# Kernel tuning notes

Hardware: AMD Instinct MI355X
Metric: run time of the kernel (lower is better)

Reference implementation:

```python
import jax, jax.numpy as jnp
import numpy as np

T, B, N, D, O = 500, 64, 512, 100, 10
ALPHA = 0.1


def setup_inputs() -> dict:
    key = jax.random.key(0)
    ks = jax.random.split(key, 13)
    sN = 1.0 / np.sqrt(N)
    sD = 1.0 / np.sqrt(D)
    return {
        "X": jax.random.normal(ks[0], (T, B, D), jnp.float32),
        "W_rec_m1": jax.random.normal(ks[1], (N, N), jnp.float32) * sN,
        "W_rec_pmd": jax.random.normal(ks[2], (N, N), jnp.float32) * sN,
        "W_rec_s1": jax.random.normal(ks[3], (N, N), jnp.float32) * sN,
        "b_m1": jnp.zeros((N,), jnp.float32),
        "b_pmd": jnp.zeros((N,), jnp.float32),
        "b_s1": jnp.zeros((N,), jnp.float32),
        "W_pmd_m1": jax.random.normal(ks[4], (N, N), jnp.float32) * sN,
        "W_s1_m1": jax.random.normal(ks[5], (N, N), jnp.float32) * sN,
        "W_m1_pmd": jax.random.normal(ks[6], (N, N), jnp.float32) * sN,
        "W_in_pmd": jax.random.normal(ks[7], (N, D), jnp.float32) * sD,
        "W_in_s1": jax.random.normal(ks[8], (N, D), jnp.float32) * sD,
        "W_out": jax.random.normal(ks[9], (O, N), jnp.float32) * sN,
    }


def reference(X, W_rec_m1, W_rec_pmd, W_rec_s1, b_m1, b_pmd, b_s1,
              W_pmd_m1, W_s1_m1, W_m1_pmd, W_in_pmd, W_in_s1, W_out):
    a = jnp.float32(ALPHA)

    def step(carry, Xt):
        x_m1, x_pmd, x_s1, r_m1, r_pmd, r_s1 = carry
        # message passing: accumulate inputs to each region
        in_m1 = r_pmd @ W_pmd_m1.T + r_s1 @ W_s1_m1.T            # [B, N]
        in_pmd = r_m1 @ W_m1_pmd.T + Xt @ W_in_pmd.T             # [B, N]
        in_s1 = Xt @ W_in_s1.T                                   # [B, N]
        # leaky-RNN f_step per region
        x_m1 = (1 - a) * x_m1 + a * (r_m1 @ W_rec_m1.T + in_m1 + b_m1)
        x_pmd = (1 - a) * x_pmd + a * (r_pmd @ W_rec_pmd.T + in_pmd + b_pmd)
        x_s1 = (1 - a) * x_s1 + a * (r_s1 @ W_rec_s1.T + in_s1 + b_s1)
        r_m1, r_pmd, r_s1 = jnp.tanh(x_m1), jnp.tanh(x_pmd), jnp.tanh(x_s1)
        out_t = r_m1 @ W_out.T                                   # [B, O]
        return (x_m1, x_pmd, x_s1, r_m1, r_pmd, r_s1), (out_t, r_m1, r_pmd, r_s1)

    z = jnp.zeros((B, N), X.dtype)
    init = (z, z, z, z, z, z)  # zero hidden; rates[0] = tanh(0) = 0
    _, (out, r_m1, r_pmd, r_s1) = jax.lax.scan(step, init, X[1:])
    return out  # [T-1, B, O]
```

## Files before the change

kernel.cpp:

```cpp
#include <hip/hip_runtime.h>
#include <hip/hip_cooperative_groups.h>

namespace cg = cooperative_groups;

#define NT 499
#define NB 64
#define NN 512
#define ND 100
#define NO 10
#define NWAVE 16
#define KW 32
#define NWG 256

typedef float f32x2 __attribute__((ext_vector_type(2)));

#define XT_SZ   (NT * ND * NB)
#define RBUF_SZ (2 * NN * NB)
#define XT_OFF  0
#define RM_OFF  (XT_OFF + XT_SZ)
#define RP_OFF  (RM_OFF + RBUF_SZ)
#define RS_OFF  (RP_OFF + RBUF_SZ)
#define FLAG_OFF (RS_OFF + RBUF_SZ)
#define RPK_STRIDE ((NN / 2) * NB)

__device__ __forceinline__ void st_cg_u(unsigned* p, unsigned v) {
  __hip_atomic_store(p, v, __ATOMIC_RELAXED, __HIP_MEMORY_SCOPE_AGENT);
}

#define LD1(dst, base, voff, IMM) \
  asm volatile("global_load_dword %0, %1, %2 offset:" IMM " sc0 sc1" \
               : "=v"(dst) : "v"(voff), "s"(base))
#define LDR(u, base, voff) do { \
  LD1(u[0],  base, voff, "0");    LD1(u[1],  base, voff, "256");  \
  LD1(u[2],  base, voff, "512");  LD1(u[3],  base, voff, "768");  \
  LD1(u[4],  base, voff, "1024"); LD1(u[5],  base, voff, "1280"); \
  LD1(u[6],  base, voff, "1536"); LD1(u[7],  base, voff, "1792"); \
  LD1(u[8],  base, voff, "2048"); LD1(u[9],  base, voff, "2304"); \
  LD1(u[10], base, voff, "2560"); LD1(u[11], base, voff, "2816"); \
  LD1(u[12], base, voff, "3072"); LD1(u[13], base, voff, "3328"); \
  LD1(u[14], base, voff, "3584"); LD1(u[15], base, voff, "3840"); \
} while (0)

#define LD_SC(dst, addr) \
  asm volatile("global_load_dword %0, %1, off sc0 sc1" : "=v"(dst) : "v"(addr))

#define PKFMA(acc, a, w) \
  asm("v_pk_fma_f32 %0, %1, %2, %0" : "+v"(acc) : "v"(a), "s"(w))

__device__ __forceinline__ unsigned f2bf(float f) {
  unsigned u = __float_as_uint(f);
  return (u + 0x7fffu + ((u >> 16) & 1u)) >> 16;
}

__global__ void xpose_kernel(const float* __restrict__ X, float* __restrict__ XT) {
  __shared__ float tile[NB * ND];
  const int t = blockIdx.x;
  const float* src = X + (size_t)(t + 1) * NB * ND;
  for (int i = threadIdx.x; i < NB * ND; i += blockDim.x) tile[i] = src[i];
  __syncthreads();
  float* dst = XT + (size_t)t * ND * NB;
  for (int i = threadIdx.x; i < NB * ND; i += blockDim.x) {
    const int d = i >> 6, b = i & 63;
    dst[i] = tile[b * ND + d];
  }
}

__global__ void __launch_bounds__(1024, 4)
rnn_kernel(const float* __restrict__ XT,
           unsigned* __restrict__ rmPK, unsigned* __restrict__ rpPK,
           unsigned* __restrict__ rsPK,
           const float* __restrict__ W_rec_m1, const float* __restrict__ W_rec_pmd,
           const float* __restrict__ W_rec_s1,
           const float* __restrict__ b_m1, const float* __restrict__ b_pmd,
           const float* __restrict__ b_s1,
           const float* __restrict__ W_pmd_m1, const float* __restrict__ W_s1_m1,
           const float* __restrict__ W_m1_pmd, const float* __restrict__ W_in_pmd,
           const float* __restrict__ W_in_s1, const float* __restrict__ W_out,
           float* __restrict__ out,
           unsigned* __restrict__ flags, unsigned* __restrict__ gen)
{
  (void)gen;
  const int g    = blockIdx.x;
  const int grp  = g >> 4;
  const int wave = __builtin_amdgcn_readfirstlane((int)threadIdx.x >> 6);
  const int lane = (int)threadIdx.x & 63;
  const int n0 = 2 * g, n1 = 2 * g + 1;
  const int k0 = __builtin_amdgcn_readfirstlane(wave * KW);
  const int m0 = __builtin_amdgcn_readfirstlane(wave * (KW / 2));
  const int d0 = __builtin_amdgcn_readfirstlane(wave * 7);
  int dlen = ND - d0; dlen = dlen < 0 ? 0 : (dlen > 7 ? 7 : dlen);
  const bool has_out = (g < NO);
  const unsigned voff = (unsigned)lane * 4u;

  __shared__ float red[NWAVE][7][64];

  for (int i = g * (int)blockDim.x + (int)threadIdx.x; i < RPK_STRIDE;
       i += (int)(gridDim.x * blockDim.x)) {
    rmPK[i] = 0u; rpPK[i] = 0u; rsPK[i] = 0u;
  }
  if (g <= 16 && threadIdx.x == 0) flags[g * 16] = 0u;

  const float* wrm0 = W_rec_m1 + (size_t)n0 * NN + k0;
  const float* wrm1 = W_rec_m1 + (size_t)n1 * NN + k0;
  const float* wmp0 = W_m1_pmd + (size_t)n0 * NN + k0;
  const float* wmp1 = W_m1_pmd + (size_t)n1 * NN + k0;
  const float* wpm0 = W_pmd_m1 + (size_t)n0 * NN + k0;
  const float* wpm1 = W_pmd_m1 + (size_t)n1 * NN + k0;
  const float* wrp0 = W_rec_pmd + (size_t)n0 * NN + k0;
  const float* wrp1 = W_rec_pmd + (size_t)n1 * NN + k0;
  const float* wsm0 = W_s1_m1 + (size_t)n0 * NN + k0;
  const float* wsm1 = W_s1_m1 + (size_t)n1 * NN + k0;
  const float* wrs0 = W_rec_s1 + (size_t)n0 * NN + k0;
  const float* wrs1 = W_rec_s1 + (size_t)n1 * NN + k0;
  const float* wip0 = W_in_pmd + (size_t)n0 * ND + d0;
  const float* wip1 = W_in_pmd + (size_t)n1 * ND + d0;
  const float* wis0 = W_in_s1 + (size_t)n0 * ND + d0;
  const float* wis1 = W_in_s1 + (size_t)n1 * ND + d0;
  const float* wo   = W_out + (size_t)(has_out ? g : 0) * NN + k0;

  unsigned* pubPK = nullptr; float bP0 = 0.f, bP1 = 0.f;
  if (wave == 0)      { pubPK = rmPK; bP0 = b_m1[n0];  bP1 = b_m1[n1]; }
  else if (wave == 1) { pubPK = rpPK; bP0 = b_pmd[n0]; bP1 = b_pmd[n1]; }
  else if (wave == 2) { pubPK = rsPK; bP0 = b_s1[n0];  bP1 = b_s1[n1]; }
  float xP0 = 0.f, xP1 = 0.f;

  float apX0 = 0.f, apX1 = 0.f, asX0 = 0.f, asX1 = 0.f;
  {
    const float* xt = XT + d0 * NB + lane;
    for (int d = 0; d < dlen; ++d) {
      const float v = xt[d * NB];
      apX0 = fmaf(v, wip0[d], apX0);
      apX1 = fmaf(v, wip1[d], apX1);
      asX0 = fmaf(v, wis0[d], asX0);
      asX1 = fmaf(v, wis1[d], asX1);
    }
  }

  cg::this_grid().sync();

  for (int ti = 0; ti < NT; ++ti) {
    const int cur = ti & 1, nxt = cur ^ 1;
    const unsigned* bM = rmPK + cur * RPK_STRIDE + m0 * NB;
    const unsigned* bP = rpPK + cur * RPK_STRIDE + m0 * NB;
    const unsigned* bS = rsPK + cur * RPK_STRIDE + m0 * NB;

    unsigned um[16], uP[16], uS[16];
    LDR(um, bM, voff);
    LDR(uP, bP, voff);
    LDR(uS, bS, voff);
    asm volatile("s_waitcnt vmcnt(0)" ::: "memory");
    __builtin_amdgcn_sched_barrier(0);

    f32x2 vm2[16];
    #pragma unroll
    for (int j = 0; j < 16; ++j) {
      vm2[j].x = __uint_as_float(um[j] << 16);
      vm2[j].y = __uint_as_float(um[j] & 0xffff0000u);
    }

    f32x2 am0p = {0.f, 0.f}, am1p = {0.f, 0.f};
    f32x2 ap0p = {apX0, 0.f}, ap1p = {apX1, 0.f};
    f32x2 as0p = {asX0, 0.f}, as1p = {asX1, 0.f};

    #pragma unroll
    for (int j = 0; j < 16; ++j) {
      const f32x2 w0 = *(const f32x2*)(wrm0 + 2 * j);
      const f32x2 w1 = *(const f32x2*)(wrm1 + 2 * j);
      const f32x2 w2 = *(const f32x2*)(wmp0 + 2 * j);
      const f32x2 w3 = *(const f32x2*)(wmp1 + 2 * j);
      PKFMA(am0p, vm2[j], w0);
      PKFMA(am1p, vm2[j], w1);
      PKFMA(ap0p, vm2[j], w2);
      PKFMA(ap1p, vm2[j], w3);
    }
    #pragma unroll
    for (int j = 0; j < 16; ++j) {
      f32x2 v; v.x = __uint_as_float(uP[j] << 16);
               v.y = __uint_as_float(uP[j] & 0xffff0000u);
      const f32x2 w0 = *(const f32x2*)(wpm0 + 2 * j);
      const f32x2 w1 = *(const f32x2*)(wpm1 + 2 * j);
      const f32x2 w2 = *(const f32x2*)(wrp0 + 2 * j);
      const f32x2 w3 = *(const f32x2*)(wrp1 + 2 * j);
      PKFMA(am0p, v, w0);
      PKFMA(am1p, v, w1);
      PKFMA(ap0p, v, w2);
      PKFMA(ap1p, v, w3);
    }
    #pragma unroll
    for (int j = 0; j < 16; ++j) {
      f32x2 v; v.x = __uint_as_float(uS[j] << 16);
               v.y = __uint_as_float(uS[j] & 0xffff0000u);
      const f32x2 w0 = *(const f32x2*)(wsm0 + 2 * j);
      const f32x2 w1 = *(const f32x2*)(wsm1 + 2 * j);
      const f32x2 w2 = *(const f32x2*)(wrs0 + 2 * j);
      const f32x2 w3 = *(const f32x2*)(wrs1 + 2 * j);
      PKFMA(am0p, v, w0);
      PKFMA(am1p, v, w1);
      PKFMA(as0p, v, w2);
      PKFMA(as1p, v, w3);
    }

    red[wave][0][lane] = am0p.x + am0p.y;
    red[wave][1][lane] = am1p.x + am1p.y;
    red[wave][2][lane] = ap0p.x + ap0p.y;
    red[wave][3][lane] = ap1p.x + ap1p.y;
    red[wave][4][lane] = as0p.x + as0p.y;
    red[wave][5][lane] = as1p.x + as1p.y;
    __syncthreads();

    if (wave < 3) {
      float s0 = red[0][2 * wave][lane], s1 = red[0][2 * wave + 1][lane];
      #pragma unroll
      for (int w = 1; w < NWAVE; ++w) {
        s0 += red[w][2 * wave][lane];
        s1 += red[w][2 * wave + 1][lane];
      }
      xP0 = 0.9f * xP0 + 0.1f * (s0 + bP0);
      xP1 = 0.9f * xP1 + 0.1f * (s1 + bP1);
      const unsigned pk = f2bf(tanhf(xP0)) | (f2bf(tanhf(xP1)) << 16);
      st_cg_u(pubPK + nxt * RPK_STRIDE + g * NB + lane, pk);
    } else if (wave == 3 && has_out && ti >= 2) {
      float s = red[0][6][lane];
      #pragma unroll
      for (int w = 1; w < NWAVE; ++w) s += red[w][6][lane];
      out[(size_t)(ti - 2) * (NB * NO) + lane * NO + g] = s;
    }

    __syncthreads();
    const unsigned tgtc = (unsigned)(ti + 1) * 16u;
    if (threadIdx.x == 0) {
      const unsigned old = __hip_atomic_fetch_add(
          &flags[(grp + 1) * 16], 1u, __ATOMIC_RELAXED, __HIP_MEMORY_SCOPE_AGENT);
      if (old == tgtc - 1u) {
        __hip_atomic_fetch_add(&flags[0], 1u, __ATOMIC_RELAXED,
                               __HIP_MEMORY_SCOPE_AGENT);
      }
    }

    apX0 = 0.f; apX1 = 0.f; asX0 = 0.f; asX1 = 0.f;
    if (ti + 1 < NT) {
      const float* xt = XT + (size_t)(ti + 1) * ND * NB + d0 * NB + lane;
      for (int d = 0; d < dlen; ++d) {
        const float v = xt[d * NB];
        apX0 = fmaf(v, wip0[d], apX0);
        apX1 = fmaf(v, wip1[d], apX1);
        asX0 = fmaf(v, wis0[d], asX0);
        asX1 = fmaf(v, wis1[d], asX1);
      }
    }
    if (has_out) {
      f32x2 aop = {0.f, 0.f};
      #pragma unroll
      for (int j = 0; j < 16; ++j) {
        const f32x2 w = *(const f32x2*)(wo + 2 * j);
        PKFMA(aop, vm2[j], w);
      }
      red[wave][6][lane] = aop.x + aop.y;
    }

    if (threadIdx.x == 0) {
      while (__hip_atomic_load(&flags[0], __ATOMIC_RELAXED,
                               __HIP_MEMORY_SCOPE_AGENT) < tgtc)
        __builtin_amdgcn_s_sleep(1);
    }
    __syncthreads();
  }

  if (has_out) {
    if (wave == 3) {
      float s = red[0][6][lane];
      #pragma unroll
      for (int w = 1; w < NWAVE; ++w) s += red[w][6][lane];
      out[(size_t)(NT - 2) * (NB * NO) + lane * NO + g] = s;
    }
    __syncthreads();
    const unsigned* rmP = rmPK + (NT & 1) * RPK_STRIDE + m0 * NB + lane;
    unsigned um[16];
    #pragma unroll
    for (int k2 = 0; k2 < 16; ++k2) LD_SC(um[k2], rmP + k2 * NB);
    asm volatile("s_waitcnt vmcnt(0)" ::: "memory");
    __builtin_amdgcn_sched_barrier(0);
    float ao = 0.f;
    #pragma unroll
    for (int k2 = 0; k2 < 16; ++k2) {
      ao = fmaf(__uint_as_float(um[k2] << 16),         wo[2 * k2],     ao);
      ao = fmaf(__uint_as_float(um[k2] & 0xffff0000u), wo[2 * k2 + 1], ao);
    }
    red[wave][6][lane] = ao;
    __syncthreads();
    if (wave == 3) {
      float t = red[0][6][lane];
      #pragma unroll
      for (int w = 1; w < NWAVE; ++w) t += red[w][6][lane];
      out[(size_t)(NT - 1) * (NB * NO) + lane * NO + g] = t;
    }
  }
}

extern "C" void kernel_launch(void* const* d_in, const int* in_sizes, int n_in,
                              void* d_out, int out_size, void* d_ws, size_t ws_size,
                              hipStream_t stream) {
  (void)in_sizes; (void)n_in; (void)out_size; (void)ws_size;
  const float* X         = (const float*)d_in[0];
  const float* W_rec_m1  = (const float*)d_in[1];
  const float* W_rec_pmd = (const float*)d_in[2];
  const float* W_rec_s1  = (const float*)d_in[3];
  const float* b_m1      = (const float*)d_in[4];
  const float* b_pmd     = (const float*)d_in[5];
  const float* b_s1      = (const float*)d_in[6];
  const float* W_pmd_m1  = (const float*)d_in[7];
  const float* W_s1_m1   = (const float*)d_in[8];
  const float* W_m1_pmd  = (const float*)d_in[9];
  const float* W_in_pmd  = (const float*)d_in[10];
  const float* W_in_s1   = (const float*)d_in[11];
  const float* W_out     = (const float*)d_in[12];
  float* out = (float*)d_out;

  float* wsf = (float*)d_ws;
  const float* XT = wsf + XT_OFF;
  float* XTw   = wsf + XT_OFF;
  unsigned* rmPK = (unsigned*)(wsf + RM_OFF);
  unsigned* rpPK = (unsigned*)(wsf + RP_OFF);
  unsigned* rsPK = (unsigned*)(wsf + RS_OFF);
  unsigned* flags = (unsigned*)(wsf + FLAG_OFF);
  unsigned* gen   = flags + 256 * 16;

  xpose_kernel<<<NT, 256, 0, stream>>>(X, XTw);

  void* args[19];
  args[0]  = (void*)&XT;
  args[1]  = (void*)&rmPK;  args[2]  = (void*)&rpPK; args[3]  = (void*)&rsPK;
  args[4]  = (void*)&W_rec_m1; args[5] = (void*)&W_rec_pmd; args[6] = (void*)&W_rec_s1;
  args[7]  = (void*)&b_m1;  args[8]  = (void*)&b_pmd; args[9]  = (void*)&b_s1;
  args[10] = (void*)&W_pmd_m1; args[11] = (void*)&W_s1_m1; args[12] = (void*)&W_m1_pmd;
  args[13] = (void*)&W_in_pmd; args[14] = (void*)&W_in_s1; args[15] = (void*)&W_out;
  args[16] = (void*)&out;
  args[17] = (void*)&flags;
  args[18] = (void*)&gen;
  hipLaunchCooperativeKernel((const void*)rnn_kernel, dim3(NWG), dim3(1024), args, 0, stream);
}
```

Before: 3.641 ms.

## Switch recurrent matvec to fp16 packed weights and v_dot2_f32_f16

Adds a pre-pass kernel that converts the six recurrent/inter-region weight matrices and W_out to packed fp16 pairs. The published rates are now stored as fp16 pairs instead of bf16. The inner loop then uses v_dot2_f32_f16 with scalar weight operands rather than unpacking bf16 into f32 pairs and issuing v_pk_fma_f32. This removes the per-element unpack shifts and masks and halves the weight bytes loaded per step. The costs are an extra launch and the use of fp16 for both weights and activations.

```diff
diff --git a/kernel.cpp b/kernel.cpp
--- a/kernel.cpp
+++ b/kernel.cpp
@@ -12,8 +12,6 @@
 #define KW 32
 #define NWG 256
 
-typedef float f32x2 __attribute__((ext_vector_type(2)));
-
 #define XT_SZ   (NT * ND * NB)
 #define RBUF_SZ (2 * NN * NB)
 #define XT_OFF  0
@@ -21,7 +19,9 @@
 #define RP_OFF  (RM_OFF + RBUF_SZ)
 #define RS_OFF  (RP_OFF + RBUF_SZ)
 #define FLAG_OFF (RS_OFF + RBUF_SZ)
+#define WPK_OFF  (FLAG_OFF + 8192)
 #define RPK_STRIDE ((NN / 2) * NB)
+#define WMAT (NN * (NN / 2))
 
 __device__ __forceinline__ void st_cg_u(unsigned* p, unsigned v) {
   __hip_atomic_store(p, v, __ATOMIC_RELAXED, __HIP_MEMORY_SCOPE_AGENT);
@@ -44,12 +44,13 @@
 #define LD_SC(dst, addr) \
   asm volatile("global_load_dword %0, %1, off sc0 sc1" : "=v"(dst) : "v"(addr))
 
-#define PKFMA(acc, a, w) \
-  asm("v_pk_fma_f32 %0, %1, %2, %0" : "+v"(acc) : "v"(a), "s"(w))
-
-__device__ __forceinline__ unsigned f2bf(float f) {
-  unsigned u = __float_as_uint(f);
-  return (u + 0x7fffu + ((u >> 16) & 1u)) >> 16;
+#define DOT2(acc, a, w) \
+  asm("v_dot2_f32_f16 %0, %1, %2, %0" : "+v"(acc) : "v"(a), "s"(w))
+
+__device__ __forceinline__ unsigned f2h2(float a, float b) {
+  union { _Float16 h[2]; unsigned u; } cv;
+  cv.h[0] = (_Float16)a; cv.h[1] = (_Float16)b;
+  return cv.u;
 }
 
 __global__ void xpose_kernel(const float* __restrict__ X, float* __restrict__ XT) {
@@ -65,27 +66,48 @@
   }
 }
 
+__global__ void wpack_kernel(const float* __restrict__ W_rec_m1,
+                             const float* __restrict__ W_m1_pmd,
+                             const float* __restrict__ W_pmd_m1,
+                             const float* __restrict__ W_rec_pmd,
+                             const float* __restrict__ W_s1_m1,
+                             const float* __restrict__ W_rec_s1,
+                             const float* __restrict__ W_out,
+                             unsigned* __restrict__ WPK) {
+  const int idx = blockIdx.x, t = threadIdx.x;
+  const float* src; unsigned* dst;
+  if (idx < 6 * NN) {
+    const int mat = idx >> 9, row = idx & (NN - 1);
+    const float* m[6] = {W_rec_m1, W_m1_pmd, W_pmd_m1, W_rec_pmd, W_s1_m1, W_rec_s1};
+    src = m[mat] + (size_t)row * NN;
+    dst = WPK + (size_t)mat * WMAT + (size_t)row * (NN / 2);
+  } else {
+    const int row = idx - 6 * NN;
+    src = W_out + (size_t)row * NN;
+    dst = WPK + (size_t)6 * WMAT + (size_t)row * (NN / 2);
+  }
+  union { _Float16 h[2]; unsigned u; } cv;
+  cv.h[0] = (_Float16)src[2 * t];
+  cv.h[1] = (_Float16)src[2 * t + 1];
+  dst[t] = cv.u;
+}
+
 __global__ void __launch_bounds__(1024, 4)
 rnn_kernel(const float* __restrict__ XT,
            unsigned* __restrict__ rmPK, unsigned* __restrict__ rpPK,
            unsigned* __restrict__ rsPK,
-           const float* __restrict__ W_rec_m1, const float* __restrict__ W_rec_pmd,
-           const float* __restrict__ W_rec_s1,
+           const unsigned* __restrict__ WPK,
            const float* __restrict__ b_m1, const float* __restrict__ b_pmd,
            const float* __restrict__ b_s1,
-           const float* __restrict__ W_pmd_m1, const float* __restrict__ W_s1_m1,
-           const float* __restrict__ W_m1_pmd, const float* __restrict__ W_in_pmd,
-           const float* __restrict__ W_in_s1, const float* __restrict__ W_out,
+           const float* __restrict__ W_in_pmd, const float* __restrict__ W_in_s1,
            float* __restrict__ out,
-           unsigned* __restrict__ flags, unsigned* __restrict__ gen)
+           unsigned* __restrict__ flags)
 {
-  (void)gen;
   const int g    = blockIdx.x;
   const int grp  = g >> 4;
   const int wave = __builtin_amdgcn_readfirstlane((int)threadIdx.x >> 6);
   const int lane = (int)threadIdx.x & 63;
   const int n0 = 2 * g, n1 = 2 * g + 1;
-  const int k0 = __builtin_amdgcn_readfirstlane(wave * KW);
   const int m0 = __builtin_amdgcn_readfirstlane(wave * (KW / 2));
   const int d0 = __builtin_amdgcn_readfirstlane(wave * 7);
   int dlen = ND - d0; dlen = dlen < 0 ? 0 : (dlen > 7 ? 7 : dlen);
@@ -100,23 +122,24 @@
   }
   if (g <= 16 && threadIdx.x == 0) flags[g * 16] = 0u;
 
-  const float* wrm0 = W_rec_m1 + (size_t)n0 * NN + k0;
-  const float* wrm1 = W_rec_m1 + (size_t)n1 * NN + k0;
-  const float* wmp0 = W_m1_pmd + (size_t)n0 * NN + k0;
-  const float* wmp1 = W_m1_pmd + (size_t)n1 * NN + k0;
-  const float* wpm0 = W_pmd_m1 + (size_t)n0 * NN + k0;
-  const float* wpm1 = W_pmd_m1 + (size_t)n1 * NN + k0;
-  const float* wrp0 = W_rec_pmd + (size_t)n0 * NN + k0;
-  const float* wrp1 = W_rec_pmd + (size_t)n1 * NN + k0;
-  const float* wsm0 = W_s1_m1 + (size_t)n0 * NN + k0;
-  const float* wsm1 = W_s1_m1 + (size_t)n1 * NN + k0;
-  const float* wrs0 = W_rec_s1 + (size_t)n0 * NN + k0;
-  const float* wrs1 = W_rec_s1 + (size_t)n1 * NN + k0;
+  const unsigned* wrm0b = WPK + (size_t)0 * WMAT + (size_t)n0 * (NN / 2) + m0;
+  const unsigned* wrm1b = WPK + (size_t)0 * WMAT + (size_t)n1 * (NN / 2) + m0;
+  const unsigned* wmp0b = WPK + (size_t)1 * WMAT + (size_t)n0 * (NN / 2) + m0;
+  const unsigned* wmp1b = WPK + (size_t)1 * WMAT + (size_t)n1 * (NN / 2) + m0;
+  const unsigned* wpm0b = WPK + (size_t)2 * WMAT + (size_t)n0 * (NN / 2) + m0;
+  const unsigned* wpm1b = WPK + (size_t)2 * WMAT + (size_t)n1 * (NN / 2) + m0;
+  const unsigned* wrp0b = WPK + (size_t)3 * WMAT + (size_t)n0 * (NN / 2) + m0;
+  const unsigned* wrp1b = WPK + (size_t)3 * WMAT + (size_t)n1 * (NN / 2) + m0;
+  const unsigned* wsm0b = WPK + (size_t)4 * WMAT + (size_t)n0 * (NN / 2) + m0;
+  const unsigned* wsm1b = WPK + (size_t)4 * WMAT + (size_t)n1 * (NN / 2) + m0;
+  const unsigned* wrs0b = WPK + (size_t)5 * WMAT + (size_t)n0 * (NN / 2) + m0;
+  const unsigned* wrs1b = WPK + (size_t)5 * WMAT + (size_t)n1 * (NN / 2) + m0;
+  const unsigned* wob   = WPK + (size_t)6 * WMAT
+                              + (size_t)(has_out ? g : 0) * (NN / 2) + m0;
   const float* wip0 = W_in_pmd + (size_t)n0 * ND + d0;
   const float* wip1 = W_in_pmd + (size_t)n1 * ND + d0;
   const float* wis0 = W_in_s1 + (size_t)n0 * ND + d0;
   const float* wis1 = W_in_s1 + (size_t)n1 * ND + d0;
-  const float* wo   = W_out + (size_t)(has_out ? g : 0) * NN + k0;
 
   unsigned* pubPK = nullptr; float bP0 = 0.f, bP1 = 0.f;
   if (wave == 0)      { pubPK = rmPK; bP0 = b_m1[n0];  bP1 = b_m1[n1]; }
@@ -151,61 +174,34 @@
     asm volatile("s_waitcnt vmcnt(0)" ::: "memory");
     __builtin_amdgcn_sched_barrier(0);
 
-    f32x2 vm2[16];
+    float am0 = 0.f, am1 = 0.f;
+    float ap0 = apX0, ap1 = apX1, as0 = asX0, as1 = asX1;
+
     #pragma unroll
     for (int j = 0; j < 16; ++j) {
-      vm2[j].x = __uint_as_float(um[j] << 16);
-      vm2[j].y = __uint_as_float(um[j] & 0xffff0000u);
-    }
-
-    f32x2 am0p = {0.f, 0.f}, am1p = {0.f, 0.f};
-    f32x2 ap0p = {apX0, 0.f}, ap1p = {apX1, 0.f};
-    f32x2 as0p = {asX0, 0.f}, as1p = {asX1, 0.f};
-
+      DOT2(am0, um[j], wrm0b[j]);
+      DOT2(am1, um[j], wrm1b[j]);
+      DOT2(ap0, um[j], wmp0b[j]);
+      DOT2(ap1, um[j], wmp1b[j]);
+    }
     #pragma unroll
     for (int j = 0; j < 16; ++j) {
-      const f32x2 w0 = *(const f32x2*)(wrm0 + 2 * j);
-      const f32x2 w1 = *(const f32x2*)(wrm1 + 2 * j);
-      const f32x2 w2 = *(const f32x2*)(wmp0 + 2 * j);
-      const f32x2 w3 = *(const f32x2*)(wmp1 + 2 * j);
-      PKFMA(am0p, vm2[j], w0);
-      PKFMA(am1p, vm2[j], w1);
-      PKFMA(ap0p, vm2[j], w2);
-      PKFMA(ap1p, vm2[j], w3);
+      DOT2(am0, uP[j], wpm0b[j]);
+      DOT2(am1, uP[j], wpm1b[j]);
+      DOT2(ap0, uP[j], wrp0b[j]);
+      DOT2(ap1, uP[j], wrp1b[j]);
     }
     #pragma unroll
     for (int j = 0; j < 16; ++j) {
-      f32x2 v; v.x = __uint_as_float(uP[j] << 16);
-               v.y = __uint_as_float(uP[j] & 0xffff0000u);
-      const f32x2 w0 = *(const f32x2*)(wpm0 + 2 * j);
-      const f32x2 w1 = *(const f32x2*)(wpm1 + 2 * j);
-      const f32x2 w2 = *(const f32x2*)(wrp0 + 2 * j);
-      const f32x2 w3 = *(const f32x2*)(wrp1 + 2 * j);
-      PKFMA(am0p, v, w0);
-      PKFMA(am1p, v, w1);
-      PKFMA(ap0p, v, w2);
-      PKFMA(ap1p, v, w3);
-    }
-    #pragma unroll
-    for (int j = 0; j < 16; ++j) {
-      f32x2 v; v.x = __uint_as_float(uS[j] << 16);
-               v.y = __uint_as_float(uS[j] & 0xffff0000u);
-      const f32x2 w0 = *(const f32x2*)(wsm0 + 2 * j);
-      const f32x2 w1 = *(const f32x2*)(wsm1 + 2 * j);
-      const f32x2 w2 = *(const f32x2*)(wrs0 + 2 * j);
-      const f32x2 w3 = *(const f32x2*)(wrs1 + 2 * j);
-      PKFMA(am0p, v, w0);
-      PKFMA(am1p, v, w1);
-      PKFMA(as0p, v, w2);
-      PKFMA(as1p, v, w3);
-    }
-
-    red[wave][0][lane] = am0p.x + am0p.y;
-    red[wave][1][lane] = am1p.x + am1p.y;
-    red[wave][2][lane] = ap0p.x + ap0p.y;
-    red[wave][3][lane] = ap1p.x + ap1p.y;
-    red[wave][4][lane] = as0p.x + as0p.y;
-    red[wave][5][lane] = as1p.x + as1p.y;
+      DOT2(am0, uS[j], wsm0b[j]);
+      DOT2(am1, uS[j], wsm1b[j]);
+      DOT2(as0, uS[j], wrs0b[j]);
+      DOT2(as1, uS[j], wrs1b[j]);
+    }
+
+    red[wave][0][lane] = am0; red[wave][1][lane] = am1;
+    red[wave][2][lane] = ap0; red[wave][3][lane] = ap1;
+    red[wave][4][lane] = as0; red[wave][5][lane] = as1;
     __syncthreads();
 
     if (wave < 3) {
@@ -217,8 +213,8 @@
       }
       xP0 = 0.9f * xP0 + 0.1f * (s0 + bP0);
       xP1 = 0.9f * xP1 + 0.1f * (s1 + bP1);
-      const unsigned pk = f2bf(tanhf(xP0)) | (f2bf(tanhf(xP1)) << 16);
-      st_cg_u(pubPK + nxt * RPK_STRIDE + g * NB + lane, pk);
+      st_cg_u(pubPK + nxt * RPK_STRIDE + g * NB + lane,
+              f2h2(tanhf(xP0), tanhf(xP1)));
     } else if (wave == 3 && has_out && ti >= 2) {
       float s = red[0][6][lane];
       #pragma unroll
@@ -249,13 +245,10 @@
       }
     }
     if (has_out) {
-      f32x2 aop = {0.f, 0.f};
-      #pragma unroll
-      for (int j = 0; j < 16; ++j) {
-        const f32x2 w = *(const f32x2*)(wo + 2 * j);
-        PKFMA(aop, vm2[j], w);
-      }
-      red[wave][6][lane] = aop.x + aop.y;
+      float ao = 0.f;
+      #pragma unroll
+      for (int j = 0; j < 16; ++j) DOT2(ao, um[j], wob[j]);
+      red[wave][6][lane] = ao;
     }
 
     if (threadIdx.x == 0) {
@@ -282,10 +275,7 @@
     __builtin_amdgcn_sched_barrier(0);
     float ao = 0.f;
     #pragma unroll
-    for (int k2 = 0; k2 < 16; ++k2) {
-      ao = fmaf(__uint_as_float(um[k2] << 16),         wo[2 * k2],     ao);
-      ao = fmaf(__uint_as_float(um[k2] & 0xffff0000u), wo[2 * k2 + 1], ao);
-    }
+    for (int j = 0; j < 16; ++j) DOT2(ao, um[j], wob[j]);
     red[wave][6][lane] = ao;
     __syncthreads();
     if (wave == 3) {
@@ -323,19 +313,20 @@
   unsigned* rpPK = (unsigned*)(wsf + RP_OFF);
   unsigned* rsPK = (unsigned*)(wsf + RS_OFF);
   unsigned* flags = (unsigned*)(wsf + FLAG_OFF);
-  unsigned* gen   = flags + 256 * 16;
+  unsigned* WPK   = (unsigned*)(wsf + WPK_OFF);
 
   xpose_kernel<<<NT, 256, 0, stream>>>(X, XTw);
-
-  void* args[19];
+  wpack_kernel<<<6 * NN + NO, 256, 0, stream>>>(
+      W_rec_m1, W_m1_pmd, W_pmd_m1, W_rec_pmd, W_s1_m1, W_rec_s1, W_out, WPK);
+
+  const unsigned* WPKc = WPK;
+  void* args[12];
   args[0]  = (void*)&XT;
   args[1]  = (void*)&rmPK;  args[2]  = (void*)&rpPK; args[3]  = (void*)&rsPK;
-  args[4]  = (void*)&W_rec_m1; args[5] = (void*)&W_rec_pmd; args[6] = (void*)&W_rec_s1;
-  args[7]  = (void*)&b_m1;  args[8]  = (void*)&b_pmd; args[9]  = (void*)&b_s1;
-  args[10] = (void*)&W_pmd_m1; args[11] = (void*)&W_s1_m1; args[12] = (void*)&W_m1_pmd;
-  args[13] = (void*)&W_in_pmd; args[14] = (void*)&W_in_s1; args[15] = (void*)&W_out;
-  args[16] = (void*)&out;
-  args[17] = (void*)&flags;
-  args[18] = (void*)&gen;
+  args[4]  = (void*)&WPKc;
+  args[5]  = (void*)&b_m1;  args[6]  = (void*)&b_pmd; args[7]  = (void*)&b_s1;
+  args[8]  = (void*)&W_in_pmd; args[9] = (void*)&W_in_s1;
+  args[10] = (void*)&out;
+  args[11] = (void*)&flags;
   hipLaunchCooperativeKernel((const void*)rnn_kernel, dim3(NWG), dim3(1024), args, 0, stream);
 }
```

Measured after the change: 3.266 ms, median of 2. 1.11x faster.
